# Performance work log

Measured on AMD Instinct MI355X. Metric: run time of the kernel, lower is better.

## Reference

```python
import jax, jax.numpy as jnp
import numpy as np

B, C, H, W = 8, 256, 64, 64
S = H * W  # dim_spatial = 4096
DQK = 256
DV = 256


def setup_inputs() -> dict:
    key = jax.random.key(0)
    k1, k2, k3, k4, k5 = jax.random.split(key, 5)
    queries = jax.random.normal(k1, (B, DQK, H, W), dtype=jnp.float32)
    keys = jax.random.normal(k2, (B, DQK, H, W), dtype=jnp.float32)
    values = jax.random.normal(k3, (B, DV, H, W), dtype=jnp.float32)
    q_pos = jax.random.normal(k4, (1, S, DQK), dtype=jnp.float32) * 0.05  # 'random_normal' init
    k_pos = jax.random.normal(k5, (1, S, DQK), dtype=jnp.float32) * 0.05
    return {"queries": queries, "keys": keys, "values": values, "q_pos": q_pos, "k_pos": k_pos}


def reference(queries, keys, values, q_pos, k_pos):
    scale = DQK ** (-0.5)
    # NCHW -> (B, S, C)
    q = jnp.transpose(queries, (0, 2, 3, 1)).reshape(-1, S, DQK) + q_pos
    k = jnp.transpose(keys, (0, 2, 3, 1)).reshape(-1, S, DQK) + k_pos
    v = jnp.transpose(values, (0, 2, 3, 1)).reshape(-1, S, DV)
    dots = jnp.einsum('bqd,bkd->bqk', q, k) * scale  # (B, S, S)
    attn = jax.nn.softmax(dots, axis=-1)
    out = jnp.einsum('bqk,bkd->bqd', attn, v)  # (B, S, DV)
    out = jnp.transpose(out, (0, 2, 1)).reshape(values.shape)  # (B, DV, H, W)
    return out
```

## Files before the change

kernel.cpp:

```cpp
#include <hip/hip_runtime.h>
#include <hip/hip_bf16.h>

#define B_N   8
#define S_N   4096
#define D_N   256
#define QBLK  128
#define KVBLK 32
#define NCH   (S_N / KVBLK)
#define IMGSZ 16384
#define SCALE 0.0625f

typedef __attribute__((ext_vector_type(8)))  short bf16x8;
typedef __attribute__((ext_vector_type(16))) float f32x16;

__device__ __forceinline__ void async16(const char* g, char* l) {
  __builtin_amdgcn_global_load_lds(
      (const __attribute__((address_space(1))) void*)g,
      (__attribute__((address_space(3))) void*)l, 16, 0, 0);
}

__device__ __forceinline__ unsigned cvt_pk_bf16(float lo, float hi) {
  unsigned r;
  asm("v_cvt_pk_bf16_f32 %0, %1, %2" : "=v"(r) : "v"(lo), "v"(hi));
  return r;
}
__device__ __forceinline__ void swap32(unsigned& a, unsigned& b) {
  asm("v_permlane32_swap_b32 %0, %1" : "+v"(a), "+v"(b));
}
__device__ __forceinline__ float xhalf_max(float x) {
  float a = x, b = x;
  asm("" : "+v"(b));
  asm("v_permlane32_swap_b32 %0, %1" : "+v"(a), "+v"(b));
  return fmaxf(a, b);
}
__device__ __forceinline__ float xhalf_add(float x) {
  float a = x, b = x;
  asm("" : "+v"(b));
  asm("v_permlane32_swap_b32 %0, %1" : "+v"(a), "+v"(b));
  return a + b;
}

__global__ void prep_qk(const float* __restrict__ src, const float* __restrict__ pos,
                        __hip_bfloat16* __restrict__ dst, float mul) {
  __shared__ float tile[64][65];
  const int b  = blockIdx.z;
  const int s0 = blockIdx.x * 64;
  const int c0 = blockIdx.y * 64;
  const int t  = threadIdx.x;
  const int x  = t & 63;
  const int y4 = t >> 6;
  const float* sp = src + ((size_t)b * D_N + c0) * S_N + s0;
#pragma unroll
  for (int i = 0; i < 16; ++i) {
    int c = y4 + i * 4;
    tile[c][x] = sp[(size_t)c * S_N + x];
  }
  __syncthreads();
  __hip_bfloat16* dp = dst + ((size_t)b * S_N + s0) * D_N + c0;
  const float* pp = pos + (size_t)s0 * D_N + c0;
#pragma unroll
  for (int i = 0; i < 16; ++i) {
    int s = y4 + i * 4;
    float v = (tile[x][s] + pp[(size_t)s * D_N + x]) * mul;
    dp[(size_t)s * D_N + x] = __float2bfloat16(v);
  }
}

__global__ void prep_kimg(const float* __restrict__ src, const float* __restrict__ pos,
                          char* __restrict__ img) {
  __shared__ float tile[64][65];
  const int b  = blockIdx.z;
  const int s0 = blockIdx.x * 64;
  const int c0 = blockIdx.y * 64;
  const int t  = threadIdx.x;
  const int x  = t & 63;
  const int y4 = t >> 6;
  const float* sp = src + ((size_t)b * D_N + c0) * S_N + s0;
#pragma unroll
  for (int i = 0; i < 16; ++i) {
    int c = y4 + i * 4;
    tile[c][x] = sp[(size_t)c * S_N + x];
  }
  __syncthreads();
  const float* pp = pos + (size_t)s0 * D_N + c0;
#pragma unroll
  for (int i = 0; i < 16; ++i) {
    int srow = y4 + i * 4;
    int d    = c0 + x;
    float v  = tile[x][srow] + pp[(size_t)srow * D_N + x];
    int s    = s0 + srow;
    int ch   = s >> 5;
    int row  = s & 31;
    char* dst = img + ((size_t)(b * NCH + ch)) * IMGSZ + row * 512
                + (((d >> 3) ^ (row & 7)) << 4) + (d & 7) * 2;
    *reinterpret_cast<__hip_bfloat16*>(dst) = __float2bfloat16(v);
  }
}

struct alignas(16) bf8s { __hip_bfloat16 v[8]; };
__global__ void prep_vimg(const float* __restrict__ src, char* __restrict__ img) {
  const int ch = blockIdx.x;
  const int b  = blockIdx.y;
  const int t  = threadIdx.x;
  char* ib = img + ((size_t)(b * NCH + ch)) * IMGSZ;
#pragma unroll
  for (int i = 0; i < 4; ++i) {
    int idx = i * 256 + t;
    int d   = idx >> 2;
    int sp  = idx & 3;
    int sl  = sp ^ ((d >> 1) & 3);
    const float* vs = src + ((size_t)b * D_N + d) * S_N + ch * KVBLK + sl * 8;
    float4 a = *reinterpret_cast<const float4*>(vs);
    float4 c = *reinterpret_cast<const float4*>(vs + 4);
    bf8s w;
    w.v[0] = __float2bfloat16(a.x); w.v[1] = __float2bfloat16(a.y);
    w.v[2] = __float2bfloat16(a.z); w.v[3] = __float2bfloat16(a.w);
    w.v[4] = __float2bfloat16(c.x); w.v[5] = __float2bfloat16(c.y);
    w.v[6] = __float2bfloat16(c.z); w.v[7] = __float2bfloat16(c.w);
    *reinterpret_cast<bf8s*>(ib + d * 64 + sp * 16) = w;
  }
}

#define LDS_BYTES 65536

__global__ __launch_bounds__(256, 2) void attn_kernel(
    const __hip_bfloat16* __restrict__ Qb, const char* __restrict__ Kt,
    const char* __restrict__ Vt, float* __restrict__ P0,
    float2* __restrict__ mlbuf, float* __restrict__ out) {
  __shared__ __align__(16) char lds[LDS_BYTES];

  const int tid  = threadIdx.x;
  const int wave = tid >> 6;
  const int lane = tid & 63;
  const int l31  = lane & 31;
  const int h    = lane >> 5;

  const int lin = blockIdx.x;
  const int b   = lin & 7;
  const int kvh = (lin >> 3) & 1;
  const int qt  = lin >> 4;
  const int q0  = qt * QBLK + wave * 32;
  const int t0  = kvh * (NCH / 2);

  bf16x8 qf[16];
  {
    const __hip_bfloat16* qp = Qb + ((size_t)b * S_N + q0 + l31) * D_N + h * 8;
#pragma unroll
    for (int kc = 0; kc < 16; ++kc)
      qf[kc] = *reinterpret_cast<const bf16x8*>(qp + kc * 16);
  }

  f32x16 o[8];
#pragma unroll
  for (int df = 0; df < 8; ++df)
#pragma unroll
    for (int r = 0; r < 16; ++r) o[df][r] = 0.f;
  float m_ = -1e30f, l_ = 0.f;

  const char* kimgB = Kt + (size_t)b * NCH * IMGSZ;
  const char* vimgB = Vt + (size_t)b * NCH * IMGSZ;

  auto COMPUTE = [&](const char* Klds, const char* Vlds) {
    f32x16 se;
#pragma unroll
    for (int r = 0; r < 16; ++r) se[r] = 0.f;
    {
      const char* kr = Klds + l31 * 512;
      const int swz = (l31 & 7) << 4;
#pragma unroll
      for (int kc = 0; kc < 16; ++kc) {
        bf16x8 kf = *reinterpret_cast<const bf16x8*>(kr + ((kc * 32 + h * 16) ^ swz));
        se = __builtin_amdgcn_mfma_f32_32x32x16_bf16(kf, qf[kc], se, 0, 0, 0);
      }
    }

    float t8[8];
#pragma unroll
    for (int i = 0; i < 8; ++i) t8[i] = fmaxf(se[i], se[i + 8]);
    float pm = fmaxf(fmaxf(fmaxf(t8[0], t8[1]), fmaxf(t8[2], t8[3])),
                     fmaxf(fmaxf(t8[4], t8[5]), fmaxf(t8[6], t8[7])));
    float pmax = xhalf_max(pm);

    if (!__all(pmax <= m_ + 8.f)) {
      float mn = fmaxf(m_, pmax);
      float al = __expf(m_ - mn);
      m_ = mn;
      l_ *= al;
#pragma unroll
      for (int df = 0; df < 8; ++df)
#pragma unroll
        for (int r = 0; r < 16; ++r) o[df][r] *= al;
    }
#pragma unroll
    for (int r = 0; r < 16; ++r) se[r] = __expf(se[r] - m_);
    float s8[8];
#pragma unroll
    for (int i = 0; i < 8; ++i) s8[i] = se[i] + se[i + 8];
    float rs = ((s8[0] + s8[1]) + (s8[2] + s8[3])) + ((s8[4] + s8[5]) + (s8[6] + s8[7]));
    l_ += xhalf_add(rs);

    union U8 { unsigned u[4]; bf16x8 v; };
    U8 pb[2];
    {
      unsigned u0 = cvt_pk_bf16(se[0],  se[1]);
      unsigned v0 = cvt_pk_bf16(se[4],  se[5]);
      swap32(u0, v0);
      unsigned u1 = cvt_pk_bf16(se[2],  se[3]);
      unsigned v1 = cvt_pk_bf16(se[6],  se[7]);
      swap32(u1, v1);
      pb[0].u[0] = u0; pb[0].u[1] = u1; pb[0].u[2] = v0; pb[0].u[3] = v1;
      unsigned u2 = cvt_pk_bf16(se[8],  se[9]);
      unsigned v2 = cvt_pk_bf16(se[12], se[13]);
      swap32(u2, v2);
      unsigned u3 = cvt_pk_bf16(se[10], se[11]);
      unsigned v3 = cvt_pk_bf16(se[14], se[15]);
      swap32(u3, v3);
      pb[1].u[0] = u2; pb[1].u[1] = u3; pb[1].u[2] = v2; pb[1].u[3] = v3;
    }

#pragma unroll
    for (int df = 0; df < 8; ++df) {
      const int d = df * 32 + l31;
      const char* vr = Vlds + d * 64;
      const int dx = (d >> 1) & 3;
#pragma unroll
      for (int kf = 0; kf < 2; ++kf) {
        bf16x8 vf = *reinterpret_cast<const bf16x8*>(vr + (((kf * 2 + h) ^ dx) << 4));
        o[df] = __builtin_amdgcn_mfma_f32_32x32x16_bf16(vf, pb[kf].v, o[df], 0, 0, 0);
      }
    }
  };

  for (int t = 0; t < NCH / 4; ++t) {
    __syncthreads();
    {
      const int ch = t0 + 2 * t + (wave & 1);
      const char* s = (wave < 2 ? kimgB : vimgB) + (size_t)ch * IMGSZ;
      char* dstb = lds + (wave < 2 ? 0 : 32768) + (wave & 1) * 16384;
#pragma unroll
      for (int c = 0; c < 16; ++c)
        async16(s + c * 1024 + lane * 16, dstb + c * 1024);
    }
    __syncthreads();

    COMPUTE(lds,         lds + 32768);
    COMPUTE(lds + 16384, lds + 49152);
  }

  if (h == 0)
    mlbuf[(size_t)(kvh * B_N + b) * S_N + q0 + l31] = make_float2(m_, l_);
  float* pdst = (kvh ? out : P0) + (size_t)b * D_N * S_N + q0 + l31;
#pragma unroll
  for (int df = 0; df < 8; ++df)
#pragma unroll
    for (int r = 0; r < 16; ++r) {
      int d = df * 32 + (r & 3) + 8 * (r >> 2) + 4 * h;
      pdst[(size_t)d * S_N] = o[df][r];
    }
}

__global__ void merge_w(const float2* __restrict__ mlbuf, float2* __restrict__ wbuf) {
  int i = blockIdx.x * 256 + threadIdx.x;
  float2 a = mlbuf[i];
  float2 c = mlbuf[(size_t)B_N * S_N + i];
  float ms = fmaxf(a.x, c.x);
  float c0 = __expf(a.x - ms), c1 = __expf(c.x - ms);
  float inv = 1.0f / (c0 * a.y + c1 * c.y);
  wbuf[i] = make_float2(c0 * inv, c1 * inv);
}

__global__ void merge_o(const float* __restrict__ P0, const float2* __restrict__ wbuf,
                        float* __restrict__ out) {
  int i = blockIdx.x * 256 + threadIdx.x;
  float4 p0 = reinterpret_cast<const float4*>(P0)[i];
  float4 p1 = reinterpret_cast<float4*>(out)[i];
  int b  = i >> 18;
  int s4 = i & (S_N / 4 - 1);
  const float2* wb = wbuf + (size_t)b * S_N + s4 * 4;
  float2 w0 = wb[0], w1 = wb[1], w2 = wb[2], w3 = wb[3];
  float4 r;
  r.x = w0.x * p0.x + w0.y * p1.x;
  r.y = w1.x * p0.y + w1.y * p1.y;
  r.z = w2.x * p0.z + w2.y * p1.z;
  r.w = w3.x * p0.w + w3.y * p1.w;
  reinterpret_cast<float4*>(out)[i] = r;
}

extern "C" void kernel_launch(void* const* d_in, const int* in_sizes, int n_in,
                              void* d_out, int out_size, void* d_ws, size_t ws_size,
                              hipStream_t stream) {
  const float* queries = (const float*)d_in[0];
  const float* keys    = (const float*)d_in[1];
  const float* values  = (const float*)d_in[2];
  const float* q_pos   = (const float*)d_in[3];
  const float* k_pos   = (const float*)d_in[4];
  float* out = (float*)d_out;

  const size_t per = (size_t)B_N * S_N * D_N;
  __hip_bfloat16* Qb = (__hip_bfloat16*)d_ws;
  char*   Kt    = (char*)d_ws + per * 2;
  char*   Vt    = Kt + per * 2;
  float*  P0    = (float*)(Vt + per * 2);
  float2* mlbuf = (float2*)((char*)P0 + per * 4);
  float2* wbuf  = mlbuf + (size_t)2 * B_N * S_N;

  prep_qk  <<<dim3(S_N / 64, D_N / 64, B_N), 256, 0, stream>>>(queries, q_pos, Qb, SCALE);
  prep_kimg<<<dim3(S_N / 64, D_N / 64, B_N), 256, 0, stream>>>(keys,    k_pos, Kt);
  prep_vimg<<<dim3(NCH, B_N), 256, 0, stream>>>(values, Vt);
  attn_kernel<<<dim3((S_N / QBLK) * B_N * 2), 256, 0, stream>>>(Qb, Kt, Vt, P0, mlbuf, out);
  merge_w<<<dim3(B_N * S_N / 256), 256, 0, stream>>>(mlbuf, wbuf);
  merge_o<<<dim3((unsigned)(per / 4 / 256)), 256, 0, stream>>>(P0, wbuf, out);
}
```

Measured before the change: 202.3 us.

## Use exp2 with log2e folded into Q scale and fragment-major K/V LDS layout

Folds log2(e) into the Q prescale so softmax can use the raw v_exp_f32 (exp2) instruction instead of __expf, dropping the extra multiply per exponential; the rescale threshold is adjusted to match the log2 domain. It also replaces the XOR-swizzled K and V image layouts with a fragment-major layout, so each lane reads contiguous 16-byte fragments at constant offsets and the address math in the inner loops goes away. The new layout may change LDS bank-conflict behaviour compared with the swizzle.

```diff
diff --git a/kernel.cpp b/kernel.cpp
--- a/kernel.cpp
+++ b/kernel.cpp
@@ -8,7 +8,7 @@
 #define KVBLK 32
 #define NCH   (S_N / KVBLK)
 #define IMGSZ 16384
-#define SCALE 0.0625f
+#define SCALE_Q (0.0625f * 1.4426950408889634f)
 
 typedef __attribute__((ext_vector_type(8)))  short bf16x8;
 typedef __attribute__((ext_vector_type(16))) float f32x16;
@@ -38,6 +38,11 @@
   asm("" : "+v"(b));
   asm("v_permlane32_swap_b32 %0, %1" : "+v"(a), "+v"(b));
   return a + b;
+}
+__device__ __forceinline__ float exp2_fast(float x) {
+  float r;
+  asm("v_exp_f32 %0, %1" : "=v"(r) : "v"(x));
+  return r;
 }
 
 __global__ void prep_qk(const float* __restrict__ src, const float* __restrict__ pos,
@@ -90,9 +95,8 @@
     float v  = tile[x][srow] + pp[(size_t)srow * D_N + x];
     int s    = s0 + srow;
     int ch   = s >> 5;
-    int row  = s & 31;
-    char* dst = img + ((size_t)(b * NCH + ch)) * IMGSZ + row * 512
-                + (((d >> 3) ^ (row & 7)) << 4) + (d & 7) * 2;
+    char* dst = img + ((size_t)(b * NCH + ch)) * IMGSZ
+                + (d >> 4) * 1024 + (s & 31) * 32 + (d & 15) * 2;
     *reinterpret_cast<__hip_bfloat16*>(dst) = __float2bfloat16(v);
   }
 }
@@ -106,10 +110,10 @@
 #pragma unroll
   for (int i = 0; i < 4; ++i) {
     int idx = i * 256 + t;
-    int d   = idx >> 2;
-    int sp  = idx & 3;
-    int sl  = sp ^ ((d >> 1) & 3);
-    const float* vs = src + ((size_t)b * D_N + d) * S_N + ch * KVBLK + sl * 8;
+    int kf  = idx >> 9;
+    int d   = (idx >> 1) & 255;
+    int hf  = idx & 1;
+    const float* vs = src + ((size_t)b * D_N + d) * S_N + ch * KVBLK + kf * 16 + hf * 8;
     float4 a = *reinterpret_cast<const float4*>(vs);
     float4 c = *reinterpret_cast<const float4*>(vs + 4);
     bf8s w;
@@ -117,7 +121,7 @@
     w.v[2] = __float2bfloat16(a.z); w.v[3] = __float2bfloat16(a.w);
     w.v[4] = __float2bfloat16(c.x); w.v[5] = __float2bfloat16(c.y);
     w.v[6] = __float2bfloat16(c.z); w.v[7] = __float2bfloat16(c.w);
-    *reinterpret_cast<bf8s*>(ib + d * 64 + sp * 16) = w;
+    *reinterpret_cast<bf8s*>(ib + kf * 8192 + d * 32 + hf * 16) = w;
   }
 }
 
@@ -134,6 +138,7 @@
   const int lane = tid & 63;
   const int l31  = lane & 31;
   const int h    = lane >> 5;
+  const int lofs = l31 * 32 + h * 16;
 
   const int lin = blockIdx.x;
   const int b   = lin & 7;
@@ -160,17 +165,16 @@
   const char* kimgB = Kt + (size_t)b * NCH * IMGSZ;
   const char* vimgB = Vt + (size_t)b * NCH * IMGSZ;
 
-  auto COMPUTE = [&](const char* Klds, const char* Vlds) {
+  auto COMPUTE = [&](const char* Kbase, const char* Vbase) {
     f32x16 se;
 #pragma unroll
     for (int r = 0; r < 16; ++r) se[r] = 0.f;
     {
-      const char* kr = Klds + l31 * 512;
-      const int swz = (l31 & 7) << 4;
+      const char* kr = Kbase + lofs;
 #pragma unroll
       for (int kc = 0; kc < 16; ++kc) {
-        bf16x8 kf = *reinterpret_cast<const bf16x8*>(kr + ((kc * 32 + h * 16) ^ swz));
-        se = __builtin_amdgcn_mfma_f32_32x32x16_bf16(kf, qf[kc], se, 0, 0, 0);
+        bf16x8 kf8 = *reinterpret_cast<const bf16x8*>(kr + kc * 1024);
+        se = __builtin_amdgcn_mfma_f32_32x32x16_bf16(kf8, qf[kc], se, 0, 0, 0);
       }
     }
 
@@ -181,9 +185,9 @@
                      fmaxf(fmaxf(t8[4], t8[5]), fmaxf(t8[6], t8[7])));
     float pmax = xhalf_max(pm);
 
-    if (!__all(pmax <= m_ + 8.f)) {
+    if (!__all(pmax <= m_ + 11.54f)) {
       float mn = fmaxf(m_, pmax);
-      float al = __expf(m_ - mn);
+      float al = exp2_fast(m_ - mn);
       m_ = mn;
       l_ *= al;
 #pragma unroll
@@ -192,7 +196,7 @@
         for (int r = 0; r < 16; ++r) o[df][r] *= al;
     }
 #pragma unroll
-    for (int r = 0; r < 16; ++r) se[r] = __expf(se[r] - m_);
+    for (int r = 0; r < 16; ++r) se[r] = exp2_fast(se[r] - m_);
     float s8[8];
 #pragma unroll
     for (int i = 0; i < 8; ++i) s8[i] = se[i] + se[i + 8];
@@ -218,15 +222,14 @@
       pb[1].u[0] = u2; pb[1].u[1] = u3; pb[1].u[2] = v2; pb[1].u[3] = v3;
     }
 
-#pragma unroll
-    for (int df = 0; df < 8; ++df) {
-      const int d = df * 32 + l31;
-      const char* vr = Vlds + d * 64;
-      const int dx = (d >> 1) & 3;
-#pragma unroll
-      for (int kf = 0; kf < 2; ++kf) {
-        bf16x8 vf = *reinterpret_cast<const bf16x8*>(vr + (((kf * 2 + h) ^ dx) << 4));
-        o[df] = __builtin_amdgcn_mfma_f32_32x32x16_bf16(vf, pb[kf].v, o[df], 0, 0, 0);
+    {
+      const char* vr = Vbase + lofs;
+#pragma unroll
+      for (int df = 0; df < 8; ++df) {
+        bf16x8 vf0 = *reinterpret_cast<const bf16x8*>(vr + df * 1024);
+        bf16x8 vf1 = *reinterpret_cast<const bf16x8*>(vr + 8192 + df * 1024);
+        o[df] = __builtin_amdgcn_mfma_f32_32x32x16_bf16(vf0, pb[0].v, o[df], 0, 0, 0);
+        o[df] = __builtin_amdgcn_mfma_f32_32x32x16_bf16(vf1, pb[1].v, o[df], 0, 0, 0);
       }
     }
   };
@@ -264,7 +267,7 @@
   float2 a = mlbuf[i];
   float2 c = mlbuf[(size_t)B_N * S_N + i];
   float ms = fmaxf(a.x, c.x);
-  float c0 = __expf(a.x - ms), c1 = __expf(c.x - ms);
+  float c0 = exp2f(a.x - ms), c1 = exp2f(c.x - ms);
   float inv = 1.0f / (c0 * a.y + c1 * c.y);
   wbuf[i] = make_float2(c0 * inv, c1 * inv);
 }
@@ -304,7 +307,7 @@
   float2* mlbuf = (float2*)((char*)P0 + per * 4);
   float2* wbuf  = mlbuf + (size_t)2 * B_N * S_N;
 
-  prep_qk  <<<dim3(S_N / 64, D_N / 64, B_N), 256, 0, stream>>>(queries, q_pos, Qb, SCALE);
+  prep_qk  <<<dim3(S_N / 64, D_N / 64, B_N), 256, 0, stream>>>(queries, q_pos, Qb, SCALE_Q);
   prep_kimg<<<dim3(S_N / 64, D_N / 64, B_N), 256, 0, stream>>>(keys,    k_pos, Kt);
   prep_vimg<<<dim3(NCH, B_N), 256, 0, stream>>>(values, Vt);
   attn_kernel<<<dim3((S_N / QBLK) * B_N * 2), 256, 0, stream>>>(Qb, Kt, Vt, P0, mlbuf, out);
```

Result: faster. 193.5 us (-4.4%).
